# Kernel optimization log

Measured on AMD Instinct MI355X. Metric: run time of the kernel, lower is better.

The kernel has to match this reference:

```python
import jax, jax.numpy as jnp
import numpy as np

DISCOUNT_FACTOR = 0.99
ADVANTAGE_LAMBDA = 0.95
LAMBD_GRAD_SCALE = 0.5


def setup_inputs() -> dict:
    key = jax.random.key(0)
    k1, k2, k3 = jax.random.split(key, 3)
    B, T, D = 4096, 2048, 1
    values = jax.random.normal(k1, (B, T + 1, D), dtype=jnp.float32)
    rewards = jax.random.normal(k2, (B, T, D), dtype=jnp.float32)
    # binary terminal flags (float, as in the torch module: used as (1 - dones))
    dones = (jax.random.uniform(k3, (B, T, D)) < 0.02).astype(jnp.float32)
    raw_gamma = jnp.zeros((1,), dtype=jnp.float32)
    raw_lambd = jnp.zeros((T,), dtype=jnp.float32)
    return {
        "values": values,
        "rewards": rewards,
        "dones": dones,
        "raw_gamma": raw_gamma,
        "raw_lambd": raw_lambd,
        "start_idx": 0,
        "end_idx": T,
    }


def reference(values, rewards, dones, raw_gamma, raw_lambd, start_idx, end_idx):
    # dynamic gamma / lambda (sigmoid-reparameterized around the base values)
    gamma = DISCOUNT_FACTOR + (1.0 - DISCOUNT_FACTOR) * (2.0 * jax.nn.sigmoid(raw_gamma) - 1.0)
    dyn_lambd = ADVANTAGE_LAMBDA + (1.0 - ADVANTAGE_LAMBDA) * (2.0 * jax.nn.sigmoid(raw_lambd) - 1.0)
    # GradScaler(scale=0.5): forward identity, gradient scaled by 0.5
    lambd = LAMBD_GRAD_SCALE * dyn_lambd + jax.lax.stop_gradient((1.0 - LAMBD_GRAD_SCALE) * dyn_lambd)
    g = gamma[0]
    td_l = lambd[start_idx:end_idx]                      # [T]

    # time-major views for the reverse-time scan
    r_tm = jnp.moveaxis(rewards, 1, 0)                   # [T, B, D]
    d_tm = jnp.moveaxis(dones, 1, 0)                     # [T, B, D]
    vn_tm = jnp.moveaxis(values[:, 1:, :], 1, 0)         # [T, B, D] = values[t+1]

    def step(carry, x):
        sum_r, lam_ret = carry
        r, d, vn, l = x
        cont = g * (1.0 - d)
        # torch computes sum_rewards under no_grad -> stop_gradient here
        new_sum = jax.lax.stop_gradient(r + cont * (l * sum_r))
        new_lam = r + cont * ((1.0 - l) * vn + l * lam_ret)
        return (new_sum, new_lam), (new_sum, new_lam)

    init = (jnp.zeros_like(values[:, -1, :]), values[:, -1, :])
    _, (sums_tm, lams_tm) = jax.lax.scan(step, init, (r_tm, d_tm, vn_tm, td_l), reverse=True)

    lambda_returns = jnp.concatenate(
        [jnp.moveaxis(lams_tm, 0, 1), values[:, -1:, :]], axis=1
    )                                                    # [B, T+1, D]
    sum_rewards = jnp.moveaxis(sums_tm, 0, 1)            # [B, T, D] (== torch sum_rewards[:, :-1])
    return lambda_returns, sum_rewards
```

## Files before the change

kernel.cpp:

```cpp
#include <hip/hip_runtime.h>


#define TPB 256
#define EPT 8

struct Aff { float aL, aS, b; };

__device__ inline Aff compose(const Aff& L, const Aff& R) {
    Aff o;
    o.aL = fmaf(L.b, R.aL, L.aL);
    o.aS = fmaf(L.b, R.aS, L.aS);
    o.b  = L.b * R.b;
    return o;
}

typedef float f4u __attribute__((ext_vector_type(4), aligned(4)));

__global__ void lam_precompute(const float* __restrict__ raw_lambd,
                               const int* __restrict__ start_p,
                               float* __restrict__ lam, int T) {
    int t = blockIdx.x * blockDim.x + threadIdx.x;
    if (t < T) lam[t] = 0.9f + 0.1f / (1.0f + __expf(-raw_lambd[start_p[0] + t]));
}

__global__ __launch_bounds__(TPB, 6)
void td_scan_kernel(const float* __restrict__ values,
                    const float* __restrict__ rewards,
                    const float* __restrict__ dones,
                    const float* __restrict__ raw_gamma,
                    const float* __restrict__ lam_arr,
                    float* __restrict__ out,
                    int B, int T)
{
    const int b    = blockIdx.x;
    const int tid  = threadIdx.x;
    const int lane = tid & 63;
    const int wave = tid >> 6;

    __shared__ float s_wAL[TPB / 64], s_wAS[TPB / 64], s_wB[TPB / 64];
    __shared__ float s_vT;

    const float g = 0.98f + 0.02f / (1.0f + __expf(-raw_gamma[0]));

    const float* vrow = values  + (size_t)b * (T + 1);
    const float* rrow = rewards + (size_t)b * T;
    const float* drow = dones   + (size_t)b * T;
    float* lam_out = out + (size_t)b * (T + 1);
    float* sum_out = out + (size_t)B * (T + 1) + (size_t)b * T;

    const int base = tid * EPT;
    const bool full = (base + EPT) <= T;

    float r[EPT], d[EPT], l[EPT], vn[EPT];
    if (full) {
        const float4 r0 = *(const float4*)(rrow + base);
        const float4 r1 = *(const float4*)(rrow + base + 4);
        const float4 d0 = *(const float4*)(drow + base);
        const float4 d1 = *(const float4*)(drow + base + 4);
        const float4 l0 = *(const float4*)(lam_arr + base);
        const float4 l1 = *(const float4*)(lam_arr + base + 4);
        const f4u    v0 = *(const f4u*)(vrow + base + 1);
        const f4u    v1 = *(const f4u*)(vrow + base + 5);
        r[0]=r0.x; r[1]=r0.y; r[2]=r0.z; r[3]=r0.w;
        r[4]=r1.x; r[5]=r1.y; r[6]=r1.z; r[7]=r1.w;
        d[0]=d0.x; d[1]=d0.y; d[2]=d0.z; d[3]=d0.w;
        d[4]=d1.x; d[5]=d1.y; d[6]=d1.z; d[7]=d1.w;
        l[0]=l0.x; l[1]=l0.y; l[2]=l0.z; l[3]=l0.w;
        l[4]=l1.x; l[5]=l1.y; l[6]=l1.z; l[7]=l1.w;
        vn[0]=v0[0]; vn[1]=v0[1]; vn[2]=v0[2]; vn[3]=v0[3];
        vn[4]=v1[0]; vn[5]=v1[1]; vn[6]=v1[2]; vn[7]=v1[3];
    } else {
        #pragma unroll
        for (int k = 0; k < EPT; ++k) {
            const int t = base + k;
            r[k]  = (t < T) ? rrow[t]     : 0.0f;
            d[k]  = (t < T) ? drow[t]     : 1.0f;
            l[k]  = (t < T) ? lam_arr[t]  : 0.0f;
            vn[k] = (t < T) ? vrow[t + 1] : 0.0f;
        }
    }
    if (tid == 0) {
        const float vT = vrow[T];
        s_vT = vT;
        lam_out[T] = vT;
    }

    Aff M[EPT];
    #pragma unroll
    for (int k = 0; k < EPT; ++k) {
        const int t = base + k;
        if (t < T) {
            const float cont = g * (1.0f - d[k]);
            M[k].b  = cont * l[k];
            M[k].aL = fmaf(cont * (1.0f - l[k]), vn[k], r[k]);
            M[k].aS = r[k];
        } else {
            M[k].aL = 0.0f; M[k].aS = 0.0f; M[k].b = 1.0f;
        }
    }
    Aff C = M[EPT - 1];
    #pragma unroll
    for (int k = EPT - 2; k >= 0; --k) C = compose(M[k], C);

    Aff S = C;
    #pragma unroll
    for (int dlt = 1; dlt < 64; dlt <<= 1) {
        Aff oth;
        oth.aL = __shfl_down(S.aL, dlt, 64);
        oth.aS = __shfl_down(S.aS, dlt, 64);
        oth.b  = __shfl_down(S.b,  dlt, 64);
        if (lane + dlt < 64) S = compose(S, oth);
    }
    Aff E;
    E.aL = __shfl_down(S.aL, 1, 64);
    E.aS = __shfl_down(S.aS, 1, 64);
    E.b  = __shfl_down(S.b,  1, 64);
    if (lane == 63) { E.aL = 0.0f; E.aS = 0.0f; E.b = 1.0f; }

    if (lane == 0) { s_wAL[wave] = S.aL; s_wAS[wave] = S.aS; s_wB[wave] = S.b; }
    __syncthreads();

    float cL = s_vT, cS = 0.0f;
    #pragma unroll
    for (int w = TPB / 64 - 1; w >= 1; --w) {
        if (w > wave) {
            const float wb = s_wB[w];
            cL = fmaf(wb, cL, s_wAL[w]);
            cS = fmaf(wb, cS, s_wAS[w]);
        }
    }

    float xL = fmaf(E.b, cL, E.aL);
    float xS = fmaf(E.b, cS, E.aS);

    float oL[EPT], oS[EPT];
    #pragma unroll
    for (int k = EPT - 1; k >= 0; --k) {
        xL = fmaf(M[k].b, xL, M[k].aL);
        xS = fmaf(M[k].b, xS, M[k].aS);
        oL[k] = xL; oS[k] = xS;
    }

    if (full) {
        *(float4*)(sum_out + base)     = make_float4(oS[0], oS[1], oS[2], oS[3]);
        *(float4*)(sum_out + base + 4) = make_float4(oS[4], oS[5], oS[6], oS[7]);
        f4u a, c;
        a[0]=oL[0]; a[1]=oL[1]; a[2]=oL[2]; a[3]=oL[3];
        c[0]=oL[4]; c[1]=oL[5]; c[2]=oL[6]; c[3]=oL[7];
        *(f4u*)(lam_out + base)     = a;
        *(f4u*)(lam_out + base + 4) = c;
    } else {
        #pragma unroll
        for (int k = 0; k < EPT; ++k) {
            const int t = base + k;
            if (t < T) { lam_out[t] = oL[k]; sum_out[t] = oS[k]; }
        }
    }
}

extern "C" void kernel_launch(void* const* d_in, const int* in_sizes, int n_in,
                              void* d_out, int out_size, void* d_ws, size_t ws_size,
                              hipStream_t stream) {
    const float* values    = (const float*)d_in[0];
    const float* rewards   = (const float*)d_in[1];
    const float* dones     = (const float*)d_in[2];
    const float* raw_gamma = (const float*)d_in[3];
    const float* raw_lambd = (const float*)d_in[4];
    const int*   start_idx = (const int*)d_in[5];
    float* out = (float*)d_out;
    float* lam_arr = (float*)d_ws;

    const int n_values  = in_sizes[0];
    const int n_rewards = in_sizes[1];
    const int B = n_values - n_rewards;
    const int T = n_rewards / B;

    lam_precompute<<<(T + 255) / 256, 256, 0, stream>>>(raw_lambd, start_idx, lam_arr, T);
    td_scan_kernel<<<B, TPB, 0, stream>>>(values, rewards, dones, raw_gamma,
                                          lam_arr, out, B, T);
}
```

Before: 155.8 us.

## Process four rows per block with software-pipelined prefetch of the next row

Each block now handles four batch rows in sequence. It loads lambda once per block and prefetches the next row's rewards, dones and values into registers while the current row's scan runs. Shared-memory wave partials are double-buffered so each row needs a single raw barrier, and launch bounds drop from 6 to 4 waves per SIMD. This is meant to hide global-load latency and amortise per-block setup, at the cost of more registers, lower occupancy and fewer blocks.

```diff
diff --git a/kernel.cpp b/kernel.cpp
--- a/kernel.cpp
+++ b/kernel.cpp
@@ -1,8 +1,10 @@
 #include <hip/hip_runtime.h>
 
 
-#define TPB 256
-#define EPT 8
+#define TPB  256
+#define EPT  8
+#define ROWS 4
+#define NW   (TPB / 64)
 
 struct Aff { float aL, aS, b; };
 
@@ -23,7 +25,36 @@
     if (t < T) lam[t] = 0.9f + 0.1f / (1.0f + __expf(-raw_lambd[start_p[0] + t]));
 }
 
-__global__ __launch_bounds__(TPB, 6)
+__device__ inline void load_row(const float* __restrict__ vrow,
+                                const float* __restrict__ rrow,
+                                const float* __restrict__ drow,
+                                int base, int T, bool full,
+                                float* r, float* d, float* vn) {
+    if (full) {
+        const float4 r0 = *(const float4*)(rrow + base);
+        const float4 r1 = *(const float4*)(rrow + base + 4);
+        const float4 d0 = *(const float4*)(drow + base);
+        const float4 d1 = *(const float4*)(drow + base + 4);
+        const f4u    v0 = *(const f4u*)(vrow + base + 1);
+        const f4u    v1 = *(const f4u*)(vrow + base + 5);
+        r[0]=r0.x; r[1]=r0.y; r[2]=r0.z; r[3]=r0.w;
+        r[4]=r1.x; r[5]=r1.y; r[6]=r1.z; r[7]=r1.w;
+        d[0]=d0.x; d[1]=d0.y; d[2]=d0.z; d[3]=d0.w;
+        d[4]=d1.x; d[5]=d1.y; d[6]=d1.z; d[7]=d1.w;
+        vn[0]=v0[0]; vn[1]=v0[1]; vn[2]=v0[2]; vn[3]=v0[3];
+        vn[4]=v1[0]; vn[5]=v1[1]; vn[6]=v1[2]; vn[7]=v1[3];
+    } else {
+        #pragma unroll
+        for (int k = 0; k < EPT; ++k) {
+            const int t = base + k;
+            r[k]  = (t < T) ? rrow[t]     : 0.0f;
+            d[k]  = (t < T) ? drow[t]     : 1.0f;
+            vn[k] = (t < T) ? vrow[t + 1] : 0.0f;
+        }
+    }
+}
+
+__global__ __launch_bounds__(TPB, 4)
 void td_scan_kernel(const float* __restrict__ values,
                     const float* __restrict__ rewards,
                     const float* __restrict__ dones,
@@ -32,129 +63,141 @@
                     float* __restrict__ out,
                     int B, int T)
 {
-    const int b    = blockIdx.x;
     const int tid  = threadIdx.x;
     const int lane = tid & 63;
     const int wave = tid >> 6;
 
-    __shared__ float s_wAL[TPB / 64], s_wAS[TPB / 64], s_wB[TPB / 64];
-    __shared__ float s_vT;
+    __shared__ float s_wAL[2][NW], s_wAS[2][NW], s_wB[2][NW];
+    __shared__ float s_vT[2];
 
     const float g = 0.98f + 0.02f / (1.0f + __expf(-raw_gamma[0]));
-
-    const float* vrow = values  + (size_t)b * (T + 1);
-    const float* rrow = rewards + (size_t)b * T;
-    const float* drow = dones   + (size_t)b * T;
-    float* lam_out = out + (size_t)b * (T + 1);
-    float* sum_out = out + (size_t)B * (T + 1) + (size_t)b * T;
 
     const int base = tid * EPT;
     const bool full = (base + EPT) <= T;
 
-    float r[EPT], d[EPT], l[EPT], vn[EPT];
+    float l[EPT];
     if (full) {
-        const float4 r0 = *(const float4*)(rrow + base);
-        const float4 r1 = *(const float4*)(rrow + base + 4);
-        const float4 d0 = *(const float4*)(drow + base);
-        const float4 d1 = *(const float4*)(drow + base + 4);
         const float4 l0 = *(const float4*)(lam_arr + base);
         const float4 l1 = *(const float4*)(lam_arr + base + 4);
-        const f4u    v0 = *(const f4u*)(vrow + base + 1);
-        const f4u    v1 = *(const f4u*)(vrow + base + 5);
-        r[0]=r0.x; r[1]=r0.y; r[2]=r0.z; r[3]=r0.w;
-        r[4]=r1.x; r[5]=r1.y; r[6]=r1.z; r[7]=r1.w;
-        d[0]=d0.x; d[1]=d0.y; d[2]=d0.z; d[3]=d0.w;
-        d[4]=d1.x; d[5]=d1.y; d[6]=d1.z; d[7]=d1.w;
         l[0]=l0.x; l[1]=l0.y; l[2]=l0.z; l[3]=l0.w;
         l[4]=l1.x; l[5]=l1.y; l[6]=l1.z; l[7]=l1.w;
-        vn[0]=v0[0]; vn[1]=v0[1]; vn[2]=v0[2]; vn[3]=v0[3];
-        vn[4]=v1[0]; vn[5]=v1[1]; vn[6]=v1[2]; vn[7]=v1[3];
     } else {
         #pragma unroll
         for (int k = 0; k < EPT; ++k) {
             const int t = base + k;
-            r[k]  = (t < T) ? rrow[t]     : 0.0f;
-            d[k]  = (t < T) ? drow[t]     : 1.0f;
-            l[k]  = (t < T) ? lam_arr[t]  : 0.0f;
-            vn[k] = (t < T) ? vrow[t + 1] : 0.0f;
-        }
-    }
-    if (tid == 0) {
-        const float vT = vrow[T];
-        s_vT = vT;
-        lam_out[T] = vT;
-    }
-
-    Aff M[EPT];
+            l[k] = (t < T) ? lam_arr[t] : 0.0f;
+        }
+    }
+
+    const int row0 = blockIdx.x * ROWS;
+    const float* vrow = values  + (size_t)row0 * (T + 1);
+    const float* rrow = rewards + (size_t)row0 * T;
+    const float* drow = dones   + (size_t)row0 * T;
+    float* lam_out = out + (size_t)row0 * (T + 1);
+    float* sum_out = out + (size_t)B * (T + 1) + (size_t)row0 * T;
+
+    float r[EPT], d[EPT], vn[EPT];
+    float vT_pref = 0.0f;
+
+    if (row0 < B) {
+        load_row(vrow, rrow, drow, base, T, full, r, d, vn);
+        if (tid == 0) vT_pref = vrow[T];
+    }
+
     #pragma unroll
-    for (int k = 0; k < EPT; ++k) {
-        const int t = base + k;
-        if (t < T) {
-            const float cont = g * (1.0f - d[k]);
-            M[k].b  = cont * l[k];
-            M[k].aL = fmaf(cont * (1.0f - l[k]), vn[k], r[k]);
-            M[k].aS = r[k];
-        } else {
-            M[k].aL = 0.0f; M[k].aS = 0.0f; M[k].b = 1.0f;
-        }
-    }
-    Aff C = M[EPT - 1];
-    #pragma unroll
-    for (int k = EPT - 2; k >= 0; --k) C = compose(M[k], C);
-
-    Aff S = C;
-    #pragma unroll
-    for (int dlt = 1; dlt < 64; dlt <<= 1) {
-        Aff oth;
-        oth.aL = __shfl_down(S.aL, dlt, 64);
-        oth.aS = __shfl_down(S.aS, dlt, 64);
-        oth.b  = __shfl_down(S.b,  dlt, 64);
-        if (lane + dlt < 64) S = compose(S, oth);
-    }
-    Aff E;
-    E.aL = __shfl_down(S.aL, 1, 64);
-    E.aS = __shfl_down(S.aS, 1, 64);
-    E.b  = __shfl_down(S.b,  1, 64);
-    if (lane == 63) { E.aL = 0.0f; E.aS = 0.0f; E.b = 1.0f; }
-
-    if (lane == 0) { s_wAL[wave] = S.aL; s_wAS[wave] = S.aS; s_wB[wave] = S.b; }
-    __syncthreads();
-
-    float cL = s_vT, cS = 0.0f;
-    #pragma unroll
-    for (int w = TPB / 64 - 1; w >= 1; --w) {
-        if (w > wave) {
-            const float wb = s_wB[w];
-            cL = fmaf(wb, cL, s_wAL[w]);
-            cS = fmaf(wb, cS, s_wAS[w]);
-        }
-    }
-
-    float xL = fmaf(E.b, cL, E.aL);
-    float xS = fmaf(E.b, cS, E.aS);
-
-    float oL[EPT], oS[EPT];
-    #pragma unroll
-    for (int k = EPT - 1; k >= 0; --k) {
-        xL = fmaf(M[k].b, xL, M[k].aL);
-        xS = fmaf(M[k].b, xS, M[k].aS);
-        oL[k] = xL; oS[k] = xS;
-    }
-
-    if (full) {
-        *(float4*)(sum_out + base)     = make_float4(oS[0], oS[1], oS[2], oS[3]);
-        *(float4*)(sum_out + base + 4) = make_float4(oS[4], oS[5], oS[6], oS[7]);
-        f4u a, c;
-        a[0]=oL[0]; a[1]=oL[1]; a[2]=oL[2]; a[3]=oL[3];
-        c[0]=oL[4]; c[1]=oL[5]; c[2]=oL[6]; c[3]=oL[7];
-        *(f4u*)(lam_out + base)     = a;
-        *(f4u*)(lam_out + base + 4) = c;
-    } else {
+    for (int j = 0; j < ROWS; ++j) {
+        const int p = j & 1;
+        const bool have = (row0 + j) < B;
+
+        Aff M[EPT];
         #pragma unroll
         for (int k = 0; k < EPT; ++k) {
             const int t = base + k;
-            if (t < T) { lam_out[t] = oL[k]; sum_out[t] = oS[k]; }
-        }
+            if (have && t < T) {
+                const float cont = g * (1.0f - d[k]);
+                M[k].b  = cont * l[k];
+                M[k].aL = fmaf(cont * (1.0f - l[k]), vn[k], r[k]);
+                M[k].aS = r[k];
+            } else {
+                M[k].aL = 0.0f; M[k].aS = 0.0f; M[k].b = 1.0f;
+            }
+        }
+
+        if (have && tid == 0) {
+            s_vT[p] = vT_pref;
+            lam_out[T] = vT_pref;
+        }
+
+        vrow += (T + 1); rrow += T; drow += T;
+        if ((j + 1 < ROWS) && ((row0 + j + 1) < B)) {
+            load_row(vrow, rrow, drow, base, T, full, r, d, vn);
+            if (tid == 0) vT_pref = vrow[T];
+        }
+
+        Aff C = M[EPT - 1];
+        #pragma unroll
+        for (int k = EPT - 2; k >= 0; --k) C = compose(M[k], C);
+
+        Aff S = C;
+        #pragma unroll
+        for (int dlt = 1; dlt < 64; dlt <<= 1) {
+            Aff oth;
+            oth.aL = __shfl_down(S.aL, dlt, 64);
+            oth.aS = __shfl_down(S.aS, dlt, 64);
+            oth.b  = __shfl_down(S.b,  dlt, 64);
+            if (lane + dlt < 64) S = compose(S, oth);
+        }
+        Aff E;
+        E.aL = __shfl_down(S.aL, 1, 64);
+        E.aS = __shfl_down(S.aS, 1, 64);
+        E.b  = __shfl_down(S.b,  1, 64);
+        if (lane == 63) { E.aL = 0.0f; E.aS = 0.0f; E.b = 1.0f; }
+
+        if (lane == 0) { s_wAL[p][wave] = S.aL; s_wAS[p][wave] = S.aS; s_wB[p][wave] = S.b; }
+
+        asm volatile("s_waitcnt lgkmcnt(0)" ::: "memory");
+        __builtin_amdgcn_s_barrier();
+        asm volatile("" ::: "memory");
+
+        if (have) {
+            float cL = s_vT[p], cS = 0.0f;
+            #pragma unroll
+            for (int w = NW - 1; w >= 1; --w) {
+                if (w > wave) {
+                    const float wb = s_wB[p][w];
+                    cL = fmaf(wb, cL, s_wAL[p][w]);
+                    cS = fmaf(wb, cS, s_wAS[p][w]);
+                }
+            }
+
+            float xL = fmaf(E.b, cL, E.aL);
+            float xS = fmaf(E.b, cS, E.aS);
+
+            float oL[EPT], oS[EPT];
+            #pragma unroll
+            for (int k = EPT - 1; k >= 0; --k) {
+                xL = fmaf(M[k].b, xL, M[k].aL);
+                xS = fmaf(M[k].b, xS, M[k].aS);
+                oL[k] = xL; oS[k] = xS;
+            }
+
+            if (full) {
+                *(float4*)(sum_out + base)     = make_float4(oS[0], oS[1], oS[2], oS[3]);
+                *(float4*)(sum_out + base + 4) = make_float4(oS[4], oS[5], oS[6], oS[7]);
+                f4u a, c;
+                a[0]=oL[0]; a[1]=oL[1]; a[2]=oL[2]; a[3]=oL[3];
+                c[0]=oL[4]; c[1]=oL[5]; c[2]=oL[6]; c[3]=oL[7];
+                *(f4u*)(lam_out + base)     = a;
+                *(f4u*)(lam_out + base + 4) = c;
+            } else {
+                #pragma unroll
+                for (int k = 0; k < EPT; ++k) {
+                    const int t = base + k;
+                    if (t < T) { lam_out[t] = oL[k]; sum_out[t] = oS[k]; }
+                }
+            }
+        }
+        lam_out += (T + 1); sum_out += T;
     }
 }
 
@@ -176,6 +219,7 @@
     const int T = n_rewards / B;
 
     lam_precompute<<<(T + 255) / 256, 256, 0, stream>>>(raw_lambd, start_idx, lam_arr, T);
-    td_scan_kernel<<<B, TPB, 0, stream>>>(values, rewards, dones, raw_gamma,
-                                          lam_arr, out, B, T);
-}
+    const int nblk = (B + ROWS - 1) / ROWS;
+    td_scan_kernel<<<nblk, TPB, 0, stream>>>(values, rewards, dones, raw_gamma,
+                                             lam_arr, out, B, T);
+}
```

Result: no change. 157.7 us (+1.2%).
